# Kernel tuning notes

Measured on AMD Instinct MI355X. Metric: run time of the kernel, lower is better.

Reference implementation:

```python
import jax, jax.numpy as jnp
import numpy as np
import math

B, L, DM, DI, DS, DR, K, NL = 1, 1024, 768, 1536, 16, 48, 4, 2
DT_MIN, DT_MAX = 0.001, 0.1


def rmsnorm(x, w, eps=1e-5):
    return x * jax.lax.rsqrt(jnp.mean(x * x, axis=-1, keepdims=True) + eps) * w


def causal_dwconv(x, w, b):
    # x: [B,L,C], w: [C,1,K]. torch Conv1d(padding=K-1)[..., :L] == left-pad K-1 causal conv.
    y = jax.lax.conv_general_dilated(
        x.transpose(0, 2, 1), w, (1,), [(K - 1, 0)],
        dimension_numbers=('NCH', 'OIH', 'NCH'), feature_group_count=DI)
    return y.transpose(0, 2, 1) + b


def selective_scan(x, delta, A, Bm, Cm, D):
    # x, delta: [B,L,DI]; A: [DI,DS]; Bm, Cm: [B,L,DS]; D: [DI]
    dA = jnp.exp(delta[..., None] * A)               # [B,L,DI,DS]
    BX = (delta * x)[..., None] * Bm[:, :, None, :]  # [B,L,DI,DS]

    def comb(c1, c2):
        a1, b1 = c1
        a2, b2 = c2
        return (a1 * a2, a2 * b1 + b2)

    _, hs = jax.lax.associative_scan(comb, (dA, BX), axis=1)  # h_t = dA_t*h_{t-1} + BX_t
    return jnp.einsum('bldn,bln->bld', hs, Cm) + D * x


def ssm(x, xproj_w, dt_w, dt_b, A_log, D):
    dbc = jnp.einsum('bld,ed->ble', x, xproj_w)            # [B,L,DR+2*DS]
    dlt, Bm, Cm = jnp.split(dbc, [DR, DR + DS], axis=-1)
    delta = jax.nn.softplus(jnp.einsum('blr,dr->bld', dlt, dt_w) + dt_b)
    return selective_scan(x, delta, -jnp.exp(A_log), Bm, Cm, D)


def mamba_block(x, p):
    xz = jnp.einsum('bld,ed->ble', x, p['in_w'])           # [B,L,2*DI]
    xin, z = jnp.split(xz, 2, axis=-1)
    xf = jax.nn.silu(causal_dwconv(xin, p['cf_w'], p['cf_b']))
    xb = jax.nn.silu(causal_dwconv(xin[:, ::-1, :], p['cb_w'], p['cb_b']))
    yf = ssm(xf, p['xf_w'], p['dtf_w'], p['dtf_b'], p['Af'], p['Df'])
    yb = ssm(xb, p['xb_w'], p['dtb_w'], p['dtb_b'], p['Ab'], p['Db'])  # NOT flipped back (faithful)
    y = jnp.einsum('ble,de->bld', jnp.concatenate([yf, yb], axis=-1), p['pro_w']) + p['pro_b']
    # tokenizer: scores over L, softmax along L, mix values; dropout = identity (eval)
    att = jax.nn.softmax(jnp.einsum('bld,td->btl', y, p['wA']), axis=-1)  # [B,T=L,L]
    vv = jnp.einsum('bld,de->ble', y, p['wV'])
    y = jnp.einsum('btl,ble->bte', att, vv)
    return jnp.einsum('bld,od->blo', y * jax.nn.silu(z), p['out_w'])


def reference(x, norm_w, in_proj_w, conv_f_w, conv_f_b, conv_b_w, conv_b_b,
              xproj_f_w, xproj_b_w, dt_f_w, dt_f_b, dt_b_w, dt_b_b,
              A_log_f, D_f, A_log_b, D_b, out_w, token_wA, token_wV, pro_w, pro_b):
    for i in range(NL):
        p = dict(in_w=in_proj_w[i], cf_w=conv_f_w[i], cf_b=conv_f_b[i],
                 cb_w=conv_b_w[i], cb_b=conv_b_b[i], xf_w=xproj_f_w[i],
                 xb_w=xproj_b_w[i], dtf_w=dt_f_w[i], dtf_b=dt_f_b[i],
                 dtb_w=dt_b_w[i], dtb_b=dt_b_b[i], Af=A_log_f[i], Df=D_f[i],
                 Ab=A_log_b[i], Db=D_b[i], out_w=out_w[i], wA=token_wA[i],
                 wV=token_wV[i], pro_w=pro_w[i], pro_b=pro_b[i])
        x = x + mamba_block(rmsnorm(x, norm_w[i]), p)
    return x


def setup_inputs():
    key = jax.random.key(0)
    ks = jax.random.split(key, 16)
    rn = lambda k, sh, s=0.02: jax.random.normal(k, sh, jnp.float32) * s
    A_log = jnp.broadcast_to(jnp.log(jnp.arange(1, DS + 1, dtype=jnp.float32)), (NL, DI, DS))
    dt = jnp.exp(jax.random.uniform(ks[0], (NL, DI)) * (math.log(DT_MAX) - math.log(DT_MIN)) + math.log(DT_MIN))
    inv_dt = dt + jnp.log(-jnp.expm1(-dt))  # softplus^-1(dt)
    dt_std = DR ** -0.5
    kaiming = (2.0 / DI) ** 0.5
    return {
        'x': jax.random.normal(ks[1], (B, L, DM), jnp.float32),
        'norm_w': jnp.ones((NL, DM), jnp.float32),
        'in_proj_w': rn(ks[2], (NL, 2 * DI, DM)),
        'conv_f_w': rn(ks[3], (NL, DI, 1, K), 0.3),
        'conv_f_b': jnp.zeros((NL, DI), jnp.float32),
        'conv_b_w': rn(ks[4], (NL, DI, 1, K), 0.3),
        'conv_b_b': jnp.zeros((NL, DI), jnp.float32),
        'xproj_f_w': rn(ks[5], (NL, DR + 2 * DS, DI)),
        'xproj_b_w': rn(ks[6], (NL, DR + 2 * DS, DI)),
        'dt_f_w': jax.random.uniform(ks[7], (NL, DI, DR), jnp.float32, -dt_std, dt_std),
        'dt_f_b': inv_dt,
        'dt_b_w': jax.random.uniform(ks[8], (NL, DI, DR), jnp.float32, -dt_std, dt_std),
        'dt_b_b': inv_dt,
        'A_log_f': A_log,
        'D_f': jnp.ones((NL, DI), jnp.float32),
        'A_log_b': A_log,
        'D_b': jnp.ones((NL, DI), jnp.float32),
        'out_w': rn(ks[9], (NL, DM, DI)),
        'token_wA': rn(ks[10], (NL, L, DI), kaiming),
        'token_wV': rn(ks[11], (NL, DI, DI), kaiming),
        'pro_w': rn(ks[12], (NL, DI, 2 * DI)),
        'pro_b': jnp.zeros((NL, DI), jnp.float32),
    }
```

## Files before the change

kernel.cpp:

```cpp
#include <hip/hip_runtime.h>
#include <hip/hip_bf16.h>
#include <math.h>
#include <stdint.h>

#define LSEQ 1024
#define DMODEL 768
#define DINNER 1536
#define DSTATE 16
#define DRANK 48
#define KCONV 4
#define NLAYER 2
#define DBC 80
#define NQ 8
#define QL (LSEQ / NQ)
#define SCH 8
#define SCW 32
#define QCH (QL / SCH)

typedef unsigned short u16;
typedef __attribute__((ext_vector_type(8))) __bf16 bf16x8;
typedef __attribute__((ext_vector_type(4))) float f32x4;
typedef __attribute__((ext_vector_type(4))) unsigned short us4;

__device__ __forceinline__ u16 f2bf(float f) {
  union { float f; unsigned u; } v; v.f = f;
  unsigned r = v.u + 0x7fffu + ((v.u >> 16) & 1u);
  return (u16)(r >> 16);
}
__device__ __forceinline__ float bf2f(u16 u) {
  union { unsigned u; float f; } v; v.u = ((unsigned)u) << 16;
  return v.f;
}

__device__ __forceinline__ void gload16(const void* g, void* l) {
  auto gp = reinterpret_cast<const __attribute__((address_space(1))) uint32_t*>(
      reinterpret_cast<uintptr_t>(g));
  auto lp = reinterpret_cast<__attribute__((address_space(3))) uint32_t*>(
      reinterpret_cast<uintptr_t>(l));
  __builtin_amdgcn_global_load_lds(gp, lp, 16, 0, 0);
}

#define CV0 589824
#define CV1 (CV0 + 1179648)
#define CV2 (CV1 + 393216)
#define CV3 (CV2 + 294912)
#define WBL 12189696
__global__ __launch_bounds__(256) void cvt4_k(
    const float* __restrict__ i0, u16* __restrict__ o0, int s0o,
    const float* __restrict__ i1, u16* __restrict__ o1, int s1o,
    const float* __restrict__ i2, u16* __restrict__ o2, int s2o,
    const float* __restrict__ i3, u16* __restrict__ o3, int s3o) {
  int i = blockIdx.x * 256 + threadIdx.x;
  int lay = blockIdx.y;
  const float* in; u16* out; int off;
  if (i < CV0)      { in = i0 + (size_t)lay * s0o * 4; out = o0 + (size_t)lay * WBL; off = i; }
  else if (i < CV1) { in = i1 + (size_t)lay * s1o * 4; out = o1 + (size_t)lay * WBL; off = i - CV0; }
  else if (i < CV2) { in = i2 + (size_t)lay * s2o * 4; out = o2 + (size_t)lay * WBL; off = i - CV1; }
  else              { in = i3 + (size_t)lay * s3o * 4; out = o3 + (size_t)lay * WBL; off = i - CV2; }
  float4 v = ((const float4*)in)[off];
  us4 o; o[0] = f2bf(v.x); o[1] = f2bf(v.y); o[2] = f2bf(v.z); o[3] = f2bf(v.w);
  ((us4*)out)[off] = o;
}

__global__ __launch_bounds__(256) void transcvt_k(const float* __restrict__ in0,
                                                  u16* __restrict__ out0,
                                                  int R, int C) {
  __shared__ float t[32][33];
  const float* in = in0 + (size_t)blockIdx.z * R * C;
  u16* out = out0 + (size_t)blockIdx.z * WBL;
  int c0 = blockIdx.x * 32, r0 = blockIdx.y * 32;
  int tx = threadIdx.x & 31, ty = threadIdx.x >> 5;
  for (int i = ty; i < 32; i += 8) t[i][tx] = in[(size_t)(r0 + i) * C + c0 + tx];
  __syncthreads();
  for (int i = ty; i < 32; i += 8)
    out[(size_t)(c0 + i) * R + r0 + tx] = f2bf(t[tx][i]);
}

__global__ __launch_bounds__(256) void rmsnorm_k(const float* __restrict__ x,
                                                 const float* __restrict__ w,
                                                 u16* __restrict__ xn) {
  int row = blockIdx.x;
  int tid = threadIdx.x;
  const float* xr = x + (size_t)row * DMODEL;
  float ss = 0.f;
  for (int j = tid; j < DMODEL; j += 256) { float v = xr[j]; ss += v * v; }
  __shared__ float red[256];
  red[tid] = ss; __syncthreads();
  for (int s = 128; s > 0; s >>= 1) { if (tid < s) red[tid] += red[tid + s]; __syncthreads(); }
  float scale = rsqrtf(red[0] / (float)DMODEL + 1e-5f);
  u16* outr = xn + (size_t)row * DMODEL;
  for (int j = tid; j < DMODEL; j += 256) outr[j] = f2bf(xr[j] * scale * w[j]);
}

template<int EPI>
__global__ __launch_bounds__(256) void mgemm_k(
    const u16* __restrict__ A, int lda,
    const u16* __restrict__ B, int ldb,
    void* __restrict__ Cv, int ldc, int K,
    const float* __restrict__ bias,
    const float* __restrict__ resid, int ldr)
{
  __shared__ u16 As[2][64 * 64];
  __shared__ u16 Bs[2][64 * 64];
  const int tid = threadIdx.x;
  const int lane = tid & 63;
  const int w = tid >> 6;

  const int nbx = gridDim.x;
  int bid = blockIdx.y * nbx + blockIdx.x;
  const int nwg = nbx * gridDim.y;
  bid = (bid & 7) * (nwg >> 3) + (bid >> 3);
  const int bm = (bid / nbx) * 64;
  const int bn = (bid % nbx) * 64;

  const int srow = lane >> 3;
  const int scs = (lane & 7) ^ srow;
  const int gA = 2 * w;
  const u16* Asrc0 = A + (size_t)(bm + gA * 8 + srow) * lda + scs * 8;
  const u16* Asrc1 = Asrc0 + (size_t)8 * lda;
  const u16* Bsrc0 = B + (size_t)(bn + gA * 8 + srow) * ldb + scs * 8;
  const u16* Bsrc1 = Bsrc0 + (size_t)8 * ldb;
  const int d0 = gA * 512;
  const int d1 = d0 + 512;

  const int fr = lane & 15;
  const int fs = lane >> 4;
  const int wm = (w >> 1) * 32;
  const int wn = (w & 1) * 32;
  int aoff[2][2], boff[2][2];
#pragma unroll
  for (int i = 0; i < 2; i++)
#pragma unroll
    for (int h = 0; h < 2; h++) {
      const int g = h * 4 + fs;
      aoff[i][h] = (wm + i * 16 + fr) * 64 + (g ^ (fr & 7)) * 8;
      boff[i][h] = (wn + i * 16 + fr) * 64 + (g ^ (fr & 7)) * 8;
    }

  f32x4 acc[2][2];
#pragma unroll
  for (int i = 0; i < 2; i++)
#pragma unroll
    for (int j = 0; j < 2; j++) acc[i][j] = (f32x4){0.f, 0.f, 0.f, 0.f};

#define STAGE(buf, k0) do { \
    gload16(Asrc0 + (k0), &As[buf][d0]); \
    gload16(Asrc1 + (k0), &As[buf][d1]); \
    gload16(Bsrc0 + (k0), &Bs[buf][d0]); \
    gload16(Bsrc1 + (k0), &Bs[buf][d1]); \
  } while (0)

  const int nk = K >> 6;
  STAGE(0, 0);

  for (int t = 0; t < nk; t++) {
    const int buf = t & 1;
    __syncthreads();
    if (t + 1 < nk) STAGE(buf ^ 1, (t + 1) << 6);
    const u16* As_ = As[buf];
    const u16* Bs_ = Bs[buf];
#pragma unroll
    for (int h = 0; h < 2; h++) {
      bf16x8 a0 = *reinterpret_cast<const bf16x8*>(As_ + aoff[0][h]);
      bf16x8 a1 = *reinterpret_cast<const bf16x8*>(As_ + aoff[1][h]);
      bf16x8 b0 = *reinterpret_cast<const bf16x8*>(Bs_ + boff[0][h]);
      bf16x8 b1 = *reinterpret_cast<const bf16x8*>(Bs_ + boff[1][h]);
      acc[0][0] = __builtin_amdgcn_mfma_f32_16x16x32_bf16(a0, b0, acc[0][0], 0, 0, 0);
      acc[0][1] = __builtin_amdgcn_mfma_f32_16x16x32_bf16(a0, b1, acc[0][1], 0, 0, 0);
      acc[1][0] = __builtin_amdgcn_mfma_f32_16x16x32_bf16(a1, b0, acc[1][0], 0, 0, 0);
      acc[1][1] = __builtin_amdgcn_mfma_f32_16x16x32_bf16(a1, b1, acc[1][1], 0, 0, 0);
    }
  }
#undef STAGE

#pragma unroll
  for (int i = 0; i < 2; i++) {
#pragma unroll
    for (int j = 0; j < 2; j++) {
      const int col = bn + wn + j * 16 + fr;
      const int row0 = bm + wm + i * 16 + fs * 4;
      float bv = (EPI & 1) ? bias[col] : 0.f;
#pragma unroll
      for (int r = 0; r < 4; r++) {
        float v = acc[i][j][r] + bv;
        if (EPI & 4) v += resid[(size_t)(row0 + r) * ldr + col];
        if (EPI & 16) {
          float z = (EPI & 32)
              ? bf2f(((const u16*)resid)[(size_t)(row0 + r) * ldr + col])
              : resid[(size_t)(row0 + r) * ldr + col];
          v *= z / (1.f + __expf(-z));
        }
        if (EPI & 8) ((u16*)Cv)[(size_t)(row0 + r) * ldc + col] = f2bf(v);
        else         ((float*)Cv)[(size_t)(row0 + r) * ldc + col] = v;
      }
    }
  }
}

template<int EPI>
__global__ __launch_bounds__(256) void mgemmW_k(
    const u16* __restrict__ A, int lda,
    const u16* __restrict__ B, int ldb,
    void* __restrict__ Cv, int ldc, int K,
    const float* __restrict__ bias,
    const float* __restrict__ resid, int ldr)
{
  __shared__ u16 As[2][64 * 64];
  __shared__ u16 Bs[2][128 * 64];
  const int tid = threadIdx.x;
  const int lane = tid & 63;
  const int w = tid >> 6;

  const int nbx = gridDim.x;
  int bid = blockIdx.y * nbx + blockIdx.x;
  const int nwg = nbx * gridDim.y;
  bid = (bid & 7) * (nwg >> 3) + (bid >> 3);
  const int bm = (bid / nbx) * 64;
  const int bn = (bid % nbx) * 128;

  const int srow = lane >> 3;
  const int scs = (lane & 7) ^ srow;
  const u16* Asrc0 = A + (size_t)(bm + (2 * w) * 8 + srow) * lda + scs * 8;
  const u16* Asrc1 = Asrc0 + (size_t)8 * lda;
  const int da0 = (2 * w) * 512, da1 = da0 + 512;
  const u16* Bsrc0 = B + (size_t)(bn + (4 * w) * 8 + srow) * ldb + scs * 8;
  const u16* Bsrc1 = Bsrc0 + (size_t)8 * ldb;
  const u16* Bsrc2 = Bsrc1 + (size_t)8 * ldb;
  const u16* Bsrc3 = Bsrc2 + (size_t)8 * ldb;
  const int db0 = (4 * w) * 512;

  const int fr = lane & 15;
  const int fs = lane >> 4;
  const int wm = (w >> 1) * 32;
  const int wn = (w & 1) * 64;
  int aoff[2][2], boff[4][2];
#pragma unroll
  for (int h = 0; h < 2; h++) {
    const int g = h * 4 + fs;
    const int sw = (g ^ (fr & 7)) * 8;
#pragma unroll
    for (int i = 0; i < 2; i++) aoff[i][h] = (wm + i * 16 + fr) * 64 + sw;
#pragma unroll
    for (int j = 0; j < 4; j++) boff[j][h] = (wn + j * 16 + fr) * 64 + sw;
  }

  f32x4 acc[2][4];
#pragma unroll
  for (int i = 0; i < 2; i++)
#pragma unroll
    for (int j = 0; j < 4; j++) acc[i][j] = (f32x4){0.f, 0.f, 0.f, 0.f};

#define STAGEW(buf, k0) do { \
    gload16(Asrc0 + (k0), &As[buf][da0]); \
    gload16(Asrc1 + (k0), &As[buf][da1]); \
    gload16(Bsrc0 + (k0), &Bs[buf][db0]); \
    gload16(Bsrc1 + (k0), &Bs[buf][db0 + 512]); \
    gload16(Bsrc2 + (k0), &Bs[buf][db0 + 1024]); \
    gload16(Bsrc3 + (k0), &Bs[buf][db0 + 1536]); \
  } while (0)

  const int nk = K >> 6;
  STAGEW(0, 0);

  for (int t = 0; t < nk; t++) {
    const int buf = t & 1;
    __syncthreads();
    if (t + 1 < nk) STAGEW(buf ^ 1, (t + 1) << 6);
    const u16* As_ = As[buf];
    const u16* Bs_ = Bs[buf];
#pragma unroll
    for (int h = 0; h < 2; h++) {
      bf16x8 a0 = *reinterpret_cast<const bf16x8*>(As_ + aoff[0][h]);
      bf16x8 a1 = *reinterpret_cast<const bf16x8*>(As_ + aoff[1][h]);
#pragma unroll
      for (int j = 0; j < 4; j++) {
        bf16x8 b = *reinterpret_cast<const bf16x8*>(Bs_ + boff[j][h]);
        acc[0][j] = __builtin_amdgcn_mfma_f32_16x16x32_bf16(a0, b, acc[0][j], 0, 0, 0);
        acc[1][j] = __builtin_amdgcn_mfma_f32_16x16x32_bf16(a1, b, acc[1][j], 0, 0, 0);
      }
    }
  }
#undef STAGEW

#pragma unroll
  for (int i = 0; i < 2; i++) {
#pragma unroll
    for (int j = 0; j < 4; j++) {
      const int col = bn + wn + j * 16 + fr;
      const int row0 = bm + wm + i * 16 + fs * 4;
      float bv = (EPI & 1) ? bias[col] : 0.f;
#pragma unroll
      for (int r = 0; r < 4; r++) {
        float v = acc[i][j][r] + bv;
        if (EPI & 4) v += resid[(size_t)(row0 + r) * ldr + col];
        if (EPI & 16) {
          float z = (EPI & 32)
              ? bf2f(((const u16*)resid)[(size_t)(row0 + r) * ldr + col])
              : resid[(size_t)(row0 + r) * ldr + col];
          v *= z / (1.f + __expf(-z));
        }
        if (EPI & 8) ((u16*)Cv)[(size_t)(row0 + r) * ldc + col] = f2bf(v);
        else         ((float*)Cv)[(size_t)(row0 + r) * ldc + col] = v;
      }
    }
  }
}

__global__ __launch_bounds__(256) void svgemm_k(
    const u16* __restrict__ wA, const u16* __restrict__ ypro,
    const u16* __restrict__ wVT,
    float* __restrict__ Smat, u16* __restrict__ vvT)
{
  __shared__ u16 As[2][64 * 64];
  __shared__ u16 Bs[2][64 * 64];
  __shared__ u16 tr[4][32][33];
  const int tid = threadIdx.x;
  const int lane = tid & 63;
  const int w = tid >> 6;

  int bid = blockIdx.x;
  bid = (bid & 7) * 80 + (bid >> 3);
  const bool is_s = bid < 256;
  const u16* A;
  const u16* B;
  int bm, bn;
  if (is_s) { A = wA;   B = ypro; bm = (bid >> 4) * 64;         bn = (bid & 15) * 64; }
  else      { A = ypro; B = wVT;  bm = ((bid - 256) / 24) * 64; bn = ((bid - 256) % 24) * 64; }

  const int srow = lane >> 3;
  const int scs = (lane & 7) ^ srow;
  const int gA = 2 * w;
  const u16* Asrc0 = A + (size_t)(bm + gA * 8 + srow) * DINNER + scs * 8;
  const u16* Asrc1 = Asrc0 + (size_t)8 * DINNER;
  const u16* Bsrc0 = B + (size_t)(bn + gA * 8 + srow) * DINNER + scs * 8;
  const u16* Bsrc1 = Bsrc0 + (size_t)8 * DINNER;
  const int d0 = gA * 512;
  const int d1 = d0 + 512;

  const int fr = lane & 15;
  const int fs = lane >> 4;
  const int wm = (w >> 1) * 32;
  const int wn = (w & 1) * 32;
  int aoff[2][2], boff[2][2];
#pragma unroll
  for (int i = 0; i < 2; i++)
#pragma unroll
    for (int h = 0; h < 2; h++) {
      const int g = h * 4 + fs;
      aoff[i][h] = (wm + i * 16 + fr) * 64 + (g ^ (fr & 7)) * 8;
      boff[i][h] = (wn + i * 16 + fr) * 64 + (g ^ (fr & 7)) * 8;
    }

  f32x4 acc[2][2];
#pragma unroll
  for (int i = 0; i < 2; i++)
#pragma unroll
    for (int j = 0; j < 2; j++) acc[i][j] = (f32x4){0.f, 0.f, 0.f, 0.f};

#define STAGE(buf, k0) do { \
    gload16(Asrc0 + (k0), &As[buf][d0]); \
    gload16(Asrc1 + (k0), &As[buf][d1]); \
    gload16(Bsrc0 + (k0), &Bs[buf][d0]); \
    gload16(Bsrc1 + (k0), &Bs[buf][d1]); \
  } while (0)

  STAGE(0, 0);
  for (int t = 0; t < DINNER / 64; t++) {
    const int buf = t & 1;
    __syncthreads();
    if (t + 1 < DINNER / 64) STAGE(buf ^ 1, (t + 1) << 6);
    const u16* As_ = As[buf];
    const u16* Bs_ = Bs[buf];
#pragma unroll
    for (int h = 0; h < 2; h++) {
      bf16x8 a0 = *reinterpret_cast<const bf16x8*>(As_ + aoff[0][h]);
      bf16x8 a1 = *reinterpret_cast<const bf16x8*>(As_ + aoff[1][h]);
      bf16x8 b0 = *reinterpret_cast<const bf16x8*>(Bs_ + boff[0][h]);
      bf16x8 b1 = *reinterpret_cast<const bf16x8*>(Bs_ + boff[1][h]);
      acc[0][0] = __builtin_amdgcn_mfma_f32_16x16x32_bf16(a0, b0, acc[0][0], 0, 0, 0);
      acc[0][1] = __builtin_amdgcn_mfma_f32_16x16x32_bf16(a0, b1, acc[0][1], 0, 0, 0);
      acc[1][0] = __builtin_amdgcn_mfma_f32_16x16x32_bf16(a1, b0, acc[1][0], 0, 0, 0);
      acc[1][1] = __builtin_amdgcn_mfma_f32_16x16x32_bf16(a1, b1, acc[1][1], 0, 0, 0);
    }
  }
#undef STAGE

  if (is_s) {
#pragma unroll
    for (int i = 0; i < 2; i++)
#pragma unroll
      for (int j = 0; j < 2; j++) {
        const int col = bn + wn + j * 16 + fr;
        const int row0 = bm + wm + i * 16 + fs * 4;
#pragma unroll
        for (int r = 0; r < 4; r++)
          Smat[(size_t)(row0 + r) * LSEQ + col] = acc[i][j][r];
      }
  } else {
#pragma unroll
    for (int i = 0; i < 2; i++)
#pragma unroll
      for (int j = 0; j < 2; j++) {
        const int lr0 = i * 16 + fs * 4;
        const int lc = j * 16 + fr;
#pragma unroll
        for (int r = 0; r < 4; r++) tr[w][lr0 + r][lc] = f2bf(acc[i][j][r]);
      }
    __syncthreads();
    const int lc = lane >> 1;
    const int half = lane & 1;
    const int gcol = bn + wn + lc;
    const int grow0 = bm + wm + half * 16;
    u16* dst = vvT + (size_t)gcol * LSEQ + grow0;
#pragma unroll
    for (int q = 0; q < 4; q++) {
      us4 v;
#pragma unroll
      for (int e = 0; e < 4; e++) v[e] = tr[w][half * 16 + q * 4 + e][lc];
      *(us4*)(dst + q * 4) = v;
    }
  }
}

#define TG_R 16
#define TG_KC 96
#define TG_KS 16

__global__ __launch_bounds__(256) void thin_gemm_k(
    const u16* __restrict__ Af_, const u16* __restrict__ Ab_,
    const float* __restrict__ Bf_, const float* __restrict__ Bb_,
    float* __restrict__ partial)
{
  __shared__ u16 As[TG_R][TG_KC];
  __shared__ float Bs[80][100];
  const u16* A = blockIdx.z ? Ab_ : Af_;
  const float* B = blockIdx.z ? Bb_ : Bf_;
  float* part = partial + (size_t)blockIdx.z * TG_KS * LSEQ * DBC;
  const int tid = threadIdx.x;
  const int m0 = blockIdx.x * TG_R;
  const int ks = blockIdx.y;
  const int k0 = ks * TG_KC;

  for (int i = tid; i < 384; i += 256) {
    int r = i / 24, q = i % 24;
    *(us4*)&As[r][q * 4] = *(const us4*)(A + (size_t)(m0 + r) * DINNER + k0 + q * 4);
  }
  for (int i = tid; i < 1920; i += 256) {
    int r = i / 24, q = i % 24;
    *(float4*)&Bs[r][q * 4] = *(const float4*)(B + (size_t)r * DINNER + k0 + q * 4);
  }
  __syncthreads();

  const int r = tid >> 4;
  const int c0 = (tid & 15) * 5;
  float acc[5] = {};
  for (int k = 0; k < TG_KC; k++) {
    float a = bf2f(As[r][k]);
#pragma unroll
    for (int j = 0; j < 5; j++) acc[j] += a * Bs[c0 + j][k];
  }
  float* out = part + ((size_t)ks * LSEQ + m0 + r) * DBC + c0;
#pragma unroll
  for (int j = 0; j < 5; j++) out[j] = acc[j];
}

__global__ __launch_bounds__(256) void reduce_dbc_k(const float* __restrict__ partial,
                                                    float* __restrict__ outf,
                                                    float* __restrict__ outb) {
  int i = blockIdx.x * 256 + threadIdx.x;
  const float* part = partial + (size_t)blockIdx.y * TG_KS * LSEQ * DBC;
  float s = 0.f;
#pragma unroll
  for (int ks = 0; ks < TG_KS; ks++) s += part[(size_t)ks * (LSEQ * DBC) + i];
  (blockIdx.y ? outb : outf)[i] = s;
}

#define BM 64
#define BN 64
#define BK 16

__global__ __launch_bounds__(256) void delta_gemm_k(
    const float* __restrict__ A0, const float* __restrict__ A1,
    const float* __restrict__ B0, const float* __restrict__ B1,
    const float* __restrict__ b0, const float* __restrict__ b1,
    u16* __restrict__ C0, u16* __restrict__ C1)
{
  __shared__ float Asf[BK][BM];
  __shared__ float Bsf[BK][BN + 4];
  const float* A = blockIdx.z ? A1 : A0;
  const float* B = blockIdx.z ? B1 : B0;
  const float* bias = blockIdx.z ? b1 : b0;
  u16* C = blockIdx.z ? C1 : C0;
  const int tid = threadIdx.x;
  const int bm = blockIdx.y * BM;
  const int bn = blockIdx.x * BN;
  const int ar = tid >> 2;
  const int ak = (tid & 3) << 2;
  const int ty = tid >> 4, tx = tid & 15;
  float acc[4][4] = {};

  for (int k0 = 0; k0 < DRANK; k0 += BK) {
    float4 av = *(const float4*)(A + (size_t)(bm + ar) * DBC + k0 + ak);
    float4 bv = *(const float4*)(B + (size_t)(bn + ar) * DRANK + k0 + ak);
    __syncthreads();
    Asf[ak + 0][ar] = av.x; Asf[ak + 1][ar] = av.y;
    Asf[ak + 2][ar] = av.z; Asf[ak + 3][ar] = av.w;
    Bsf[ak + 0][ar] = bv.x; Bsf[ak + 1][ar] = bv.y;
    Bsf[ak + 2][ar] = bv.z; Bsf[ak + 3][ar] = bv.w;
    __syncthreads();
#pragma unroll
    for (int kk = 0; kk < BK; kk++) {
      float4 a4 = *(const float4*)&Asf[kk][ty * 4];
      float4 b4 = *(const float4*)&Bsf[kk][tx * 4];
      float a[4] = {a4.x, a4.y, a4.z, a4.w};
      float b[4] = {b4.x, b4.y, b4.z, b4.w};
#pragma unroll
      for (int i = 0; i < 4; i++)
#pragma unroll
        for (int j = 0; j < 4; j++)
          acc[i][j] += a[i] * b[j];
    }
  }

#pragma unroll
  for (int i = 0; i < 4; i++) {
    int row = bm + ty * 4 + i;
#pragma unroll
    for (int j = 0; j < 4; j++) {
      int col = bn + tx * 4 + j;
      float v = acc[i][j] + bias[col];
      v = (v > 20.f) ? v : log1pf(__expf(v));
      C[(size_t)row * DINNER + col] = f2bf(v);
    }
  }
}

__global__ __launch_bounds__(256) void conv_silu_k(
    const u16* __restrict__ xz,
    const float* __restrict__ wf, const float* __restrict__ bf,
    const float* __restrict__ wb, const float* __restrict__ bb,
    u16* __restrict__ xf, u16* __restrict__ xb)
{
  int idx = blockIdx.x * 256 + threadIdx.x;
  int dir = blockIdx.y;
  if (idx >= LSEQ * DINNER) return;
  int l = idx / DINNER, c = idx % DINNER;
  const float* w = (dir ? wb : wf) + c * KCONV;
  float acc = (dir ? bb : bf)[c];
#pragma unroll
  for (int k = 0; k < KCONV; k++) {
    int ls = l - (KCONV - 1) + k;
    if (ls >= 0) {
      int lsrc = dir ? (LSEQ - 1 - ls) : ls;
      acc += w[k] * bf2f(xz[(size_t)lsrc * (2 * DINNER) + c]);
    }
  }
  float sv = acc / (1.f + __expf(-acc));
  (dir ? xb : xf)[idx] = f2bf(sv);
}

__global__ __launch_bounds__(256) void scan_a_k(
    const u16* __restrict__ xcf, const u16* __restrict__ xcb,
    const u16* __restrict__ dltf, const u16* __restrict__ dltb,
    const float* __restrict__ dbcf, const float* __restrict__ dbcb,
    const float* __restrict__ Af, const float* __restrict__ Ab,
    float* __restrict__ qsP, float* __restrict__ qsQ)
{
  __shared__ float sP[SCH * SCW * DSTATE];
  __shared__ float sQ[SCH * SCW * DSTATE];
  const int dir = blockIdx.z;
  const int qid = blockIdx.y;
  const u16*   xc    = dir ? xcb : xcf;
  const u16*   delta = dir ? dltb : dltf;
  const float* dbc   = dir ? dbcb : dbcf;
  const float* A_log = dir ? Ab : Af;

  const int tid = threadIdx.x;
  const int c = tid >> 5;
  const int dl = tid & 31;
  const int d = blockIdx.x * SCW + dl;

  float Aa[DSTATE];
#pragma unroll
  for (int s = 0; s < DSTATE; s++) Aa[s] = -__expf(A_log[(size_t)d * DSTATE + s]);
  const float Aa0 = Aa[0];
  bool fast = true;
#pragma unroll
  for (int s = 1; s < DSTATE; s++)
    fast = fast && (fabsf(Aa[s] - Aa0 * (float)(s + 1)) <= 1e-4f * fabsf(Aa[s]));

  float aP[DSTATE], q[DSTATE];
#pragma unroll
  for (int s = 0; s < DSTATE; s++) { aP[s] = 1.f; q[s] = 0.f; }
  const int l0 = qid * QL + c * QCH;
  if (fast) {
    for (int i = 0; i < QCH; i++) {
      int l = l0 + i;
      float dt = bf2f(delta[(size_t)l * DINNER + d]);
      float dx = dt * bf2f(xc[(size_t)l * DINNER + d]);
      const float* bm = dbc + (size_t)l * DBC + DRANK;
      float e0 = __expf(dt * Aa0);
      float a = 1.f;
#pragma unroll
      for (int s = 0; s < DSTATE; s++) {
        a *= e0;
        q[s] = a * q[s] + dx * bm[s];
        aP[s] *= a;
      }
    }
  } else {
    for (int i = 0; i < QCH; i++) {
      int l = l0 + i;
      float dt = bf2f(delta[(size_t)l * DINNER + d]);
      float dx = dt * bf2f(xc[(size_t)l * DINNER + d]);
      const float* bm = dbc + (size_t)l * DBC + DRANK;
#pragma unroll
      for (int s = 0; s < DSTATE; s++) {
        float a = __expf(dt * Aa[s]);
        q[s] = a * q[s] + dx * bm[s];
        aP[s] *= a;
      }
    }
  }
#pragma unroll
  for (int s = 0; s < DSTATE; s++) {
    sP[(c * SCW + dl) * DSTATE + s] = aP[s];
    sQ[(c * SCW + dl) * DSTATE + s] = q[s];
  }
  __syncthreads();

#pragma unroll
  for (int pp = 0; pp < 2; pp++) {
    const int p = tid + pp * 256;
    const int d2 = p >> 4, s2 = p & 15;
    float h = 0.f, P = 1.f;
    for (int cc = 0; cc < SCH; cc++) {
      int idx = (cc * SCW + d2) * DSTATE + s2;
      h = sP[idx] * h + sQ[idx];
      P *= sP[idx];
    }
    size_t o = (((size_t)dir * NQ + qid) * DINNER + blockIdx.x * SCW + d2) * DSTATE + s2;
    qsP[o] = P;
    qsQ[o] = h;
  }
}

__global__ __launch_bounds__(256) void scan_c_k(
    const u16* __restrict__ xcf, const u16* __restrict__ xcb,
    const u16* __restrict__ dltf, const u16* __restrict__ dltb,
    const float* __restrict__ dbcf, const float* __restrict__ dbcb,
    const float* __restrict__ Af, const float* __restrict__ Ab,
    const float* __restrict__ Df, const float* __restrict__ Db,
    const float* __restrict__ qsP, const float* __restrict__ qsQ,
    u16* __restrict__ ycat)
{
  __shared__ float sP[SCH * SCW * DSTATE];
  __shared__ float sQ[SCH * SCW * DSTATE];
  const int dir = blockIdx.z;
  const int qid = blockIdx.y;
  const u16*   xc    = dir ? xcb : xcf;
  const u16*   delta = dir ? dltb : dltf;
  const float* dbc   = dir ? dbcb : dbcf;
  const float* A_log = dir ? Ab : Af;
  const float* Dvec  = dir ? Db : Df;
  const int col_off  = dir ? DINNER : 0;

  const int tid = threadIdx.x;
  const int c = tid >> 5;
  const int dl = tid & 31;
  const int d = blockIdx.x * SCW + dl;

  float Aa[DSTATE];
#pragma unroll
  for (int s = 0; s < DSTATE; s++) Aa[s] = -__expf(A_log[(size_t)d * DSTATE + s]);
  const float Aa0 = Aa[0];
  bool fast = true;
#pragma unroll
  for (int s = 1; s < DSTATE; s++)
    fast = fast && (fabsf(Aa[s] - Aa0 * (float)(s + 1)) <= 1e-4f * fabsf(Aa[s]));

  float aP[DSTATE], q[DSTATE];
#pragma unroll
  for (int s = 0; s < DSTATE; s++) { aP[s] = 1.f; q[s] = 0.f; }
  const int l0 = qid * QL + c * QCH;
  if (fast) {
    for (int i = 0; i < QCH; i++) {
      int l = l0 + i;
      float dt = bf2f(delta[(size_t)l * DINNER + d]);
      float dx = dt * bf2f(xc[(size_t)l * DINNER + d]);
      const float* bm = dbc + (size_t)l * DBC + DRANK;
      float e0 = __expf(dt * Aa0);
      float a = 1.f;
#pragma unroll
      for (int s = 0; s < DSTATE; s++) {
        a *= e0;
        q[s] = a * q[s] + dx * bm[s];
        aP[s] *= a;
      }
    }
  } else {
    for (int i = 0; i < QCH; i++) {
      int l = l0 + i;
      float dt = bf2f(delta[(size_t)l * DINNER + d]);
      float dx = dt * bf2f(xc[(size_t)l * DINNER + d]);
      const float* bm = dbc + (size_t)l * DBC + DRANK;
#pragma unroll
      for (int s = 0; s < DSTATE; s++) {
        float a = __expf(dt * Aa[s]);
        q[s] = a * q[s] + dx * bm[s];
        aP[s] *= a;
      }
    }
  }
#pragma unroll
  for (int s = 0; s < DSTATE; s++) {
    sP[(c * SCW + dl) * DSTATE + s] = aP[s];
    sQ[(c * SCW + dl) * DSTATE + s] = q[s];
  }
  __syncthreads();

#pragma unroll
  for (int pp = 0; pp < 2; pp++) {
    const int p = tid + pp * 256;
    const int d2 = p >> 4, s2 = p & 15;
    float h = 0.f;
    for (int qq = 0; qq < qid; qq++) {
      size_t o = (((size_t)dir * NQ + qq) * DINNER + blockIdx.x * SCW + d2) * DSTATE + s2;
      h = qsP[o] * h + qsQ[o];
    }
    for (int cc = 0; cc < SCH; cc++) {
      int idx = (cc * SCW + d2) * DSTATE + s2;
      float a = sP[idx], qv = sQ[idx];
      sP[idx] = h;
      h = a * h + qv;
    }
  }
  __syncthreads();

  float hs[DSTATE];
#pragma unroll
  for (int s = 0; s < DSTATE; s++) hs[s] = sP[(c * SCW + dl) * DSTATE + s];
  const float Dd = Dvec[d];
  if (fast) {
    for (int i = 0; i < QCH; i++) {
      int l = l0 + i;
      float dt = bf2f(delta[(size_t)l * DINNER + d]);
      float xv = bf2f(xc[(size_t)l * DINNER + d]);
      float dx = dt * xv;
      const float* bm = dbc + (size_t)l * DBC + DRANK;
      const float* cm = bm + DSTATE;
      float e0 = __expf(dt * Aa0);
      float a = 1.f;
      float y = 0.f;
#pragma unroll
      for (int s = 0; s < DSTATE; s++) {
        a *= e0;
        hs[s] = a * hs[s] + dx * bm[s];
        y += hs[s] * cm[s];
      }
      ycat[(size_t)l * (2 * DINNER) + col_off + d] = f2bf(y + Dd * xv);
    }
  } else {
    for (int i = 0; i < QCH; i++) {
      int l = l0 + i;
      float dt = bf2f(delta[(size_t)l * DINNER + d]);
      float xv = bf2f(xc[(size_t)l * DINNER + d]);
      float dx = dt * xv;
      const float* bm = dbc + (size_t)l * DBC + DRANK;
      const float* cm = bm + DSTATE;
      float y = 0.f;
#pragma unroll
      for (int s = 0; s < DSTATE; s++) {
        float a = __expf(dt * Aa[s]);
        hs[s] = a * hs[s] + dx * bm[s];
        y += hs[s] * cm[s];
      }
      ycat[(size_t)l * (2 * DINNER) + col_off + d] = f2bf(y + Dd * xv);
    }
  }
}

__global__ __launch_bounds__(256) void softmax_k(const float* __restrict__ S,
                                                 u16* __restrict__ P) {
  int row = blockIdx.x, tid = threadIdx.x;
  __shared__ float buf[LSEQ];
  __shared__ float red[256];
  const float* r = S + (size_t)row * LSEQ;
  float m = -1e30f;
  for (int j = tid; j < LSEQ; j += 256) { float v = r[j]; buf[j] = v; m = fmaxf(m, v); }
  red[tid] = m; __syncthreads();
  for (int s = 128; s > 0; s >>= 1) { if (tid < s) red[tid] = fmaxf(red[tid], red[tid + s]); __syncthreads(); }
  m = red[0];
  __syncthreads();
  float sum = 0.f;
  for (int j = tid; j < LSEQ; j += 256) { float e = __expf(buf[j] - m); buf[j] = e; sum += e; }
  red[tid] = sum; __syncthreads();
  for (int s = 128; s > 0; s >>= 1) { if (tid < s) red[tid] += red[tid + s]; __syncthreads(); }
  float inv = 1.f / red[0];
  u16* pr = P + (size_t)row * LSEQ;
  for (int j = tid; j < LSEQ; j += 256) pr[j] = f2bf(buf[j] * inv);
}

extern "C" void kernel_launch(void* const* d_in, const int* in_sizes, int n_in,
                              void* d_out, int out_size, void* d_ws, size_t ws_size,
                              hipStream_t stream) {
  const float* in_x      = (const float*)d_in[0];
  const float* norm_w    = (const float*)d_in[1];
  const float* in_proj_w = (const float*)d_in[2];
  const float* conv_f_w  = (const float*)d_in[3];
  const float* conv_f_b  = (const float*)d_in[4];
  const float* conv_b_w  = (const float*)d_in[5];
  const float* conv_b_b  = (const float*)d_in[6];
  const float* xproj_f_w = (const float*)d_in[7];
  const float* xproj_b_w = (const float*)d_in[8];
  const float* dt_f_w    = (const float*)d_in[9];
  const float* dt_f_b    = (const float*)d_in[10];
  const float* dt_b_w    = (const float*)d_in[11];
  const float* dt_b_b    = (const float*)d_in[12];
  const float* A_log_f   = (const float*)d_in[13];
  const float* D_f       = (const float*)d_in[14];
  const float* A_log_b   = (const float*)d_in[15];
  const float* D_b       = (const float*)d_in[16];
  const float* out_w     = (const float*)d_in[17];
  const float* token_wA  = (const float*)d_in[18];
  const float* token_wV  = (const float*)d_in[19];
  const float* pro_w     = (const float*)d_in[20];
  const float* pro_b     = (const float*)d_in[21];

  float* ws = (float*)d_ws;
  float* xbuf = ws; ws += LSEQ * DMODEL;
  u16* xz_bf  = (u16*)ws; ws += LSEQ * DINNER;
  u16* xf_bf  = (u16*)ws; ws += (LSEQ * DINNER) / 2;
  u16* xb_bf  = (u16*)ws; ws += (LSEQ * DINNER) / 2;
  float* dbcf = ws; ws += LSEQ * DBC;
  float* dbcb = ws; ws += LSEQ * DBC;
  float* delf_r = ws; ws += LSEQ * DINNER;
  float* delb_r = ws; ws += LSEQ * DINNER;
  float* scr  = ws; ws += LSEQ * DINNER;
  u16* xn_bf   = (u16*)ws; ws += (LSEQ * DMODEL) / 2;
  u16* ycat_bf = (u16*)ws; ws += LSEQ * DINNER;
  u16* ypro_bf = (u16*)ws; ws += (LSEQ * DINNER) / 2;
  u16* Wb      = (u16*)ws;

  u16* in_w_bf0 = Wb;
  u16* pw_bf0   = in_w_bf0 + 3072 * 768;
  u16* wA_bf0   = pw_bf0 + 1536 * 3072;
  u16* wVT_bf0  = wA_bf0 + 1024 * 1536;
  u16* ow_bf0   = wVT_bf0 + 1536 * 1536;

  float* dbc_part = delf_r;
  u16*   delf_bf  = (u16*)delf_r;
  u16*   delb_bf  = (u16*)delb_r;
  float* Smat     = delf_r;
  u16*   Smat_bf  = (u16*)delb_r;
  u16*   vvT_bf   = xb_bf;
  u16*   g_bf     = ypro_bf;
  const int QS = 2 * NQ * DINNER * DSTATE;
  float* qsP   = scr;
  float* qsQ   = scr + QS;

  dim3 blk(256);

  cvt4_k<<<dim3(CV3 / 256, NLAYER), blk, 0, stream>>>(
      in_proj_w, in_w_bf0, 2 * DINNER * DMODEL / 4,
      pro_w,     pw_bf0,   DINNER * 2 * DINNER / 4,
      token_wA,  wA_bf0,   LSEQ * DINNER / 4,
      out_w,     ow_bf0,   DMODEL * DINNER / 4);
  transcvt_k<<<dim3(1536 / 32, 1536 / 32, NLAYER), blk, 0, stream>>>(
      token_wV, wVT_bf0, 1536, 1536);

  for (int layer = 0; layer < NLAYER; layer++) {
    const float* nw  = norm_w    + (size_t)layer * DMODEL;
    const float* cfw = conv_f_w  + (size_t)layer * DINNER * KCONV;
    const float* cfb = conv_f_b  + (size_t)layer * DINNER;
    const float* cbw = conv_b_w  + (size_t)layer * DINNER * KCONV;
    const float* cbb = conv_b_b  + (size_t)layer * DINNER;
    const float* xfw = xproj_f_w + (size_t)layer * DBC * DINNER;
    const float* xbw = xproj_b_w + (size_t)layer * DBC * DINNER;
    const float* dfw = dt_f_w    + (size_t)layer * DINNER * DRANK;
    const float* dfb = dt_f_b    + (size_t)layer * DINNER;
    const float* dbw = dt_b_w    + (size_t)layer * DINNER * DRANK;
    const float* dbb = dt_b_b    + (size_t)layer * DINNER;
    const float* Af  = A_log_f   + (size_t)layer * DINNER * DSTATE;
    const float* Df  = D_f       + (size_t)layer * DINNER;
    const float* Ab  = A_log_b   + (size_t)layer * DINNER * DSTATE;
    const float* Db  = D_b       + (size_t)layer * DINNER;
    const float* pb  = pro_b     + (size_t)layer * DINNER;

    u16* in_w_bf = in_w_bf0 + (size_t)layer * WBL;
    u16* pw_bf   = pw_bf0   + (size_t)layer * WBL;
    u16* wA_bf   = wA_bf0   + (size_t)layer * WBL;
    u16* wVT_bf  = wVT_bf0  + (size_t)layer * WBL;
    u16* ow_bf   = ow_bf0   + (size_t)layer * WBL;

    const float* xsrc = (layer == 0) ? in_x : xbuf;

    rmsnorm_k<<<LSEQ, blk, 0, stream>>>(xsrc, nw, xn_bf);

    mgemmW_k<8><<<dim3(3072 / 128, LSEQ / 64), blk, 0, stream>>>(
        xn_bf, DMODEL, in_w_bf, DMODEL, xz_bf, 2 * DINNER, DMODEL, nullptr, nullptr, 0);

    conv_silu_k<<<dim3((LSEQ * DINNER) / 256, 2), blk, 0, stream>>>(
        xz_bf, cfw, cfb, cbw, cbb, xf_bf, xb_bf);

    thin_gemm_k<<<dim3(LSEQ / TG_R, TG_KS, 2), blk, 0, stream>>>(
        xf_bf, xb_bf, xfw, xbw, dbc_part);
    reduce_dbc_k<<<dim3((LSEQ * DBC) / 256, 2), blk, 0, stream>>>(
        dbc_part, dbcf, dbcb);

    delta_gemm_k<<<dim3(DINNER / BN, LSEQ / BM, 2), blk, 0, stream>>>(
        dbcf, dbcb, dfw, dbw, dfb, dbb, delf_bf, delb_bf);

    scan_a_k<<<dim3(DINNER / SCW, NQ - 1, 2), blk, 0, stream>>>(
        xf_bf, xb_bf, delf_bf, delb_bf, dbcf, dbcb, Af, Ab, qsP, qsQ);
    scan_c_k<<<dim3(DINNER / SCW, NQ, 2), blk, 0, stream>>>(
        xf_bf, xb_bf, delf_bf, delb_bf, dbcf, dbcb, Af, Ab, Df, Db, qsP, qsQ, ycat_bf);

    mgemmW_k<9><<<dim3(DINNER / 128, LSEQ / 64), blk, 0, stream>>>(
        ycat_bf, 2 * DINNER, pw_bf, 2 * DINNER, ypro_bf, DINNER, 2 * DINNER,
        pb, nullptr, 0);

    svgemm_k<<<640, blk, 0, stream>>>(wA_bf, ypro_bf, wVT_bf, Smat, vvT_bf);
    softmax_k<<<LSEQ, blk, 0, stream>>>(Smat, Smat_bf);

    mgemmW_k<56><<<dim3(DINNER / 128, LSEQ / 64), blk, 0, stream>>>(
        Smat_bf, LSEQ, vvT_bf, LSEQ, g_bf, DINNER, LSEQ,
        nullptr, (const float*)(xz_bf + DINNER), 2 * DINNER);

    float* target = (layer == NLAYER - 1) ? (float*)d_out : xbuf;
    mgemm_k<4><<<dim3(DMODEL / 64, LSEQ / 64), blk, 0, stream>>>(
        g_bf, DINNER, ow_bf, DINNER, target, DMODEL, DINNER,
        nullptr, xsrc, DMODEL);
  }
}
```

Before: 398.5 us.

## Store per-subchunk scan states in bf16 to avoid recomputing local scan

scan_a now writes each subchunk's decay product and partial state in bf16, for all quarters, directly to global memory. scan_c loads these into shared memory instead of redoing the chunk-local recurrence with its exponentials. The cross-chunk prefix in scan_c now walks every subchunk state from global memory. This removes duplicated exp/FMA work in scan_c. In exchange it adds more global traffic and bf16 rounding of the intermediate scan states, which may hurt accuracy.

New measurement: 404.0 us. Within noise of the previous version (+1.4%).

```diff
diff --git a/kernel.cpp b/kernel.cpp
--- a/kernel.cpp
+++ b/kernel.cpp
@@ -564,16 +564,15 @@
     const u16* __restrict__ dltf, const u16* __restrict__ dltb,
     const float* __restrict__ dbcf, const float* __restrict__ dbcb,
     const float* __restrict__ Af, const float* __restrict__ Ab,
-    float* __restrict__ qsP, float* __restrict__ qsQ)
+    u16* __restrict__ cP, u16* __restrict__ cQf_, u16* __restrict__ cQb_)
 {
-  __shared__ float sP[SCH * SCW * DSTATE];
-  __shared__ float sQ[SCH * SCW * DSTATE];
   const int dir = blockIdx.z;
   const int qid = blockIdx.y;
   const u16*   xc    = dir ? xcb : xcf;
   const u16*   delta = dir ? dltb : dltf;
   const float* dbc   = dir ? dbcb : dbcf;
   const float* A_log = dir ? Ab : Af;
+  u16* cQ = dir ? cQb_ : cQf_;
 
   const int tid = threadIdx.x;
   const int c = tid >> 5;
@@ -622,26 +621,12 @@
       }
     }
   }
+  const size_t bp = ((((size_t)dir * NQ + qid) * SCH + c) * DINNER + d) * DSTATE;
+  const size_t bq = (((size_t)qid * SCH + c) * DINNER + d) * DSTATE;
 #pragma unroll
   for (int s = 0; s < DSTATE; s++) {
-    sP[(c * SCW + dl) * DSTATE + s] = aP[s];
-    sQ[(c * SCW + dl) * DSTATE + s] = q[s];
-  }
-  __syncthreads();
-
-#pragma unroll
-  for (int pp = 0; pp < 2; pp++) {
-    const int p = tid + pp * 256;
-    const int d2 = p >> 4, s2 = p & 15;
-    float h = 0.f, P = 1.f;
-    for (int cc = 0; cc < SCH; cc++) {
-      int idx = (cc * SCW + d2) * DSTATE + s2;
-      h = sP[idx] * h + sQ[idx];
-      P *= sP[idx];
-    }
-    size_t o = (((size_t)dir * NQ + qid) * DINNER + blockIdx.x * SCW + d2) * DSTATE + s2;
-    qsP[o] = P;
-    qsQ[o] = h;
+    cP[bp + s] = f2bf(aP[s]);
+    cQ[bq + s] = f2bf(q[s]);
   }
 }
 
@@ -651,7 +636,8 @@
     const float* __restrict__ dbcf, const float* __restrict__ dbcb,
     const float* __restrict__ Af, const float* __restrict__ Ab,
     const float* __restrict__ Df, const float* __restrict__ Db,
-    const float* __restrict__ qsP, const float* __restrict__ qsQ,
+    const u16* __restrict__ cP, const u16* __restrict__ cQf_,
+    const u16* __restrict__ cQb_,
     u16* __restrict__ ycat)
 {
   __shared__ float sP[SCH * SCW * DSTATE];
@@ -663,12 +649,22 @@
   const float* dbc   = dir ? dbcb : dbcf;
   const float* A_log = dir ? Ab : Af;
   const float* Dvec  = dir ? Db : Df;
+  const u16*   cQ    = dir ? cQb_ : cQf_;
   const int col_off  = dir ? DINNER : 0;
 
   const int tid = threadIdx.x;
   const int c = tid >> 5;
   const int dl = tid & 31;
-  const int d = blockIdx.x * SCW + dl;
+  const int bx = blockIdx.x;
+  const int d = bx * SCW + dl;
+
+  for (int i = tid; i < SCH * SCW * DSTATE; i += 256) {
+    const int cc = i >> 9, rem = i & 511, d2 = rem >> 4, s2 = rem & 15;
+    const size_t gp = ((((size_t)dir * NQ + qid) * SCH + cc) * DINNER + bx * SCW + d2) * DSTATE + s2;
+    const size_t gq = (((size_t)qid * SCH + cc) * DINNER + bx * SCW + d2) * DSTATE + s2;
+    sP[i] = bf2f(cP[gp]);
+    sQ[i] = bf2f(cQ[gq]);
+  }
 
   float Aa[DSTATE];
 #pragma unroll
@@ -678,45 +674,6 @@
 #pragma unroll
   for (int s = 1; s < DSTATE; s++)
     fast = fast && (fabsf(Aa[s] - Aa0 * (float)(s + 1)) <= 1e-4f * fabsf(Aa[s]));
-
-  float aP[DSTATE], q[DSTATE];
-#pragma unroll
-  for (int s = 0; s < DSTATE; s++) { aP[s] = 1.f; q[s] = 0.f; }
-  const int l0 = qid * QL + c * QCH;
-  if (fast) {
-    for (int i = 0; i < QCH; i++) {
-      int l = l0 + i;
-      float dt = bf2f(delta[(size_t)l * DINNER + d]);
-      float dx = dt * bf2f(xc[(size_t)l * DINNER + d]);
-      const float* bm = dbc + (size_t)l * DBC + DRANK;
-      float e0 = __expf(dt * Aa0);
-      float a = 1.f;
-#pragma unroll
-      for (int s = 0; s < DSTATE; s++) {
-        a *= e0;
-        q[s] = a * q[s] + dx * bm[s];
-        aP[s] *= a;
-      }
-    }
-  } else {
-    for (int i = 0; i < QCH; i++) {
-      int l = l0 + i;
-      float dt = bf2f(delta[(size_t)l * DINNER + d]);
-      float dx = dt * bf2f(xc[(size_t)l * DINNER + d]);
-      const float* bm = dbc + (size_t)l * DBC + DRANK;
-#pragma unroll
-      for (int s = 0; s < DSTATE; s++) {
-        float a = __expf(dt * Aa[s]);
-        q[s] = a * q[s] + dx * bm[s];
-        aP[s] *= a;
-      }
-    }
-  }
-#pragma unroll
-  for (int s = 0; s < DSTATE; s++) {
-    sP[(c * SCW + dl) * DSTATE + s] = aP[s];
-    sQ[(c * SCW + dl) * DSTATE + s] = q[s];
-  }
   __syncthreads();
 
 #pragma unroll
@@ -725,12 +682,16 @@
     const int d2 = p >> 4, s2 = p & 15;
     float h = 0.f;
     for (int qq = 0; qq < qid; qq++) {
-      size_t o = (((size_t)dir * NQ + qq) * DINNER + blockIdx.x * SCW + d2) * DSTATE + s2;
-      h = qsP[o] * h + qsQ[o];
+#pragma unroll
+      for (int cc = 0; cc < SCH; cc++) {
+        const size_t gp = ((((size_t)dir * NQ + qq) * SCH + cc) * DINNER + bx * SCW + d2) * DSTATE + s2;
+        const size_t gq = (((size_t)qq * SCH + cc) * DINNER + bx * SCW + d2) * DSTATE + s2;
+        h = bf2f(cP[gp]) * h + bf2f(cQ[gq]);
+      }
     }
     for (int cc = 0; cc < SCH; cc++) {
-      int idx = (cc * SCW + d2) * DSTATE + s2;
-      float a = sP[idx], qv = sQ[idx];
+      const int idx = (cc * SCW + d2) * DSTATE + s2;
+      const float a = sP[idx], qv = sQ[idx];
       sP[idx] = h;
       h = a * h + qv;
     }
@@ -741,6 +702,7 @@
 #pragma unroll
   for (int s = 0; s < DSTATE; s++) hs[s] = sP[(c * SCW + dl) * DSTATE + s];
   const float Dd = Dvec[d];
+  const int l0 = qid * QL + c * QCH;
   if (fast) {
     for (int i = 0; i < QCH; i++) {
       int l = l0 + i;
@@ -851,13 +813,13 @@
   float* dbc_part = delf_r;
   u16*   delf_bf  = (u16*)delf_r;
   u16*   delb_bf  = (u16*)delb_r;
+  u16*   cQf      = (u16*)(delf_r + (LSEQ * DINNER) / 2);
+  u16*   cQb      = (u16*)(delb_r + (LSEQ * DINNER) / 2);
+  u16*   cP       = (u16*)scr;
   float* Smat     = delf_r;
   u16*   Smat_bf  = (u16*)delb_r;
   u16*   vvT_bf   = xb_bf;
   u16*   g_bf     = ypro_bf;
-  const int QS = 2 * NQ * DINNER * DSTATE;
-  float* qsP   = scr;
-  float* qsQ   = scr + QS;
 
   dim3 blk(256);
 
@@ -911,10 +873,11 @@
     delta_gemm_k<<<dim3(DINNER / BN, LSEQ / BM, 2), blk, 0, stream>>>(
         dbcf, dbcb, dfw, dbw, dfb, dbb, delf_bf, delb_bf);
 
-    scan_a_k<<<dim3(DINNER / SCW, NQ - 1, 2), blk, 0, stream>>>(
-        xf_bf, xb_bf, delf_bf, delb_bf, dbcf, dbcb, Af, Ab, qsP, qsQ);
+    scan_a_k<<<dim3(DINNER / SCW, NQ, 2), blk, 0, stream>>>(
+        xf_bf, xb_bf, delf_bf, delb_bf, dbcf, dbcb, Af, Ab, cP, cQf, cQb);
     scan_c_k<<<dim3(DINNER / SCW, NQ, 2), blk, 0, stream>>>(
-        xf_bf, xb_bf, delf_bf, delb_bf, dbcf, dbcb, Af, Ab, Df, Db, qsP, qsQ, ycat_bf);
+        xf_bf, xb_bf, delf_bf, delb_bf, dbcf, dbcb, Af, Ab, Df, Db,
+        cP, cQf, cQb, ycat_bf);
 
     mgemmW_k<9><<<dim3(DINNER / 128, LSEQ / 64), blk, 0, stream>>>(
         ycat_bf, 2 * DINNER, pw_bf, 2 * DINNER, ypro_bf, DINNER, 2 * DINNER,
```
